# Kernel tuning notes

Measured on AMD Instinct MI355X. Metric: run time of the kernel, lower is better.

## Reference

```python
import jax, jax.numpy as jnp
import numpy as np

N = 16384          # num_nodes
B = 2              # batch_size
F = 32             # feature_size (hard-coded in module)
G = 16             # num_gru_units
OUT = 16           # output_dim


def _normalized_laplacian(adj):
    # calculate_laplacian_with_self_loop: D^-1/2 (A + I) D^-1/2
    a = adj + jnp.eye(adj.shape[0], dtype=adj.dtype)
    d = a.sum(axis=1)
    dinv = jax.lax.rsqrt(d)
    return dinv[:, None] * a * dinv[None, :]


def setup_inputs() -> dict:
    key = jax.random.key(0)
    k1, k2, k3, k4 = jax.random.split(key, 4)
    adj = (jax.random.uniform(k1, (N, N), dtype=jnp.float32) < 0.01).astype(jnp.float32)
    laplacian = _normalized_laplacian(adj)
    inputs = jax.random.normal(k2, (B, N, F), dtype=jnp.float32)
    hidden_state = jax.random.normal(k3, (B, N * G), dtype=jnp.float32)
    # xavier_uniform for weights [(G+F), OUT]
    limit = np.sqrt(6.0 / (G + F + OUT)).astype(np.float32)
    weights = jax.random.uniform(k4, (G + F, OUT), dtype=jnp.float32, minval=-limit, maxval=limit)
    biases = jnp.zeros((OUT,), dtype=jnp.float32)
    return {"inputs": inputs, "hidden_state": hidden_state, "laplacian": laplacian,
            "weights": weights, "biases": biases}


def reference(inputs, hidden_state, laplacian, weights, biases):
    b, n, f = inputs.shape
    g = weights.shape[0] - f
    out_dim = weights.shape[1]
    h = hidden_state.reshape(b, n, g)
    cat = jnp.concatenate([inputs, h], axis=2)              # [B, N, F+G]
    # laplacian @ concat over the node dimension (same math as the
    # reshape/transpose dance + per-batch sparse GEMM loop in the original)
    ax = jnp.einsum('mn,bnc->bmc', laplacian, cat)          # [B, N, F+G]
    out = ax @ weights + biases                             # [B, N, OUT]
    return out.reshape(b, n * out_dim)
```

## Files before the change

### kernel.cpp

```cpp
#include <hip/hip_runtime.h>
#include <hip/hip_bf16.h>


#define NN   16384
#define FF   32
#define GG   16
#define OUTD 16
#define C96  96
#define BM   64
#define BK   128
#define SPLITK 2
#define KCHUNK (NN / SPLITK)
#define KITERS (KCHUNK / BK)

typedef __attribute__((ext_vector_type(8))) short short8;
typedef __attribute__((ext_vector_type(4))) float f32x4;

using as1_void = __attribute__((address_space(1))) void;
using as3_void = __attribute__((address_space(3))) void;

__device__ __forceinline__ unsigned short f2bf(float f) {
  __hip_bfloat16 h = __float2bfloat16(f);
  return __builtin_bit_cast(unsigned short, h);
}

__global__ __launch_bounds__(256) void prep_xt(const float* __restrict__ inp,
                                               const float* __restrict__ hid,
                                               unsigned short* __restrict__ xt) {
  __shared__ float lds_cat[C96][64];
  const int tid = threadIdx.x;
  const int n0 = blockIdx.x * 64;

#pragma unroll
  for (int r = 0; r < 2; ++r) {
    int fi = tid + r * 256;
    int n = fi >> 3;
    int f4 = fi & 7;
#pragma unroll
    for (int b = 0; b < 2; ++b) {
      const float4* src = (const float4*)(inp + ((size_t)b * NN + (n0 + n)) * FF) + f4;
      float4 v = *src;
      int c = b * 48 + f4 * 4;
      lds_cat[c + 0][n] = v.x;
      lds_cat[c + 1][n] = v.y;
      lds_cat[c + 2][n] = v.z;
      lds_cat[c + 3][n] = v.w;
    }
  }
  {
    int n = tid >> 2;
    int g4 = tid & 3;
#pragma unroll
    for (int b = 0; b < 2; ++b) {
      const float4* src = (const float4*)(hid + ((size_t)b * NN + (n0 + n)) * GG) + g4;
      float4 v = *src;
      int c = b * 48 + 32 + g4 * 4;
      lds_cat[c + 0][n] = v.x;
      lds_cat[c + 1][n] = v.y;
      lds_cat[c + 2][n] = v.z;
      lds_cat[c + 3][n] = v.w;
    }
  }
  __syncthreads();
#pragma unroll
  for (int r = 0; r < 3; ++r) {
    int u = tid + r * 256;
    int c = u >> 3;
    int nn = (u & 7) * 8;
    short8 o;
#pragma unroll
    for (int j = 0; j < 8; ++j) o[j] = (short)f2bf(lds_cat[c][nn + j]);
    *(short8*)(xt + (size_t)c * NN + n0 + nn) = o;
  }
}

__global__ __launch_bounds__(256, 2) void spmm_main(const float* __restrict__ L,
                                                    const unsigned short* __restrict__ xt,
                                                    float* __restrict__ cp) {
  __shared__ __align__(16) float lds_a[BM * BK];
  __shared__ __align__(16) unsigned short lds_b[C96 * BK];

  const int tid = threadIdx.x;
  const int wave = tid >> 6;
  const int lane = tid & 63;
  const int m = lane & 15;
  const int quad = lane >> 4;
  const int sp = blockIdx.x & 1;
  const int m0 = (blockIdx.x >> 1) * BM;
  const int kb = sp * KCHUNK;

  const float* asrc[8];
  float* adst[8];
#pragma unroll
  for (int i = 0; i < 8; ++i) {
    int l = wave * 8 + i;
    int row = 2 * l + (lane >> 5);
    int cu = (lane & 31) ^ (row & 7);
    asrc[i] = L + (size_t)(m0 + row) * NN + kb + cu * 4;
    adst[i] = lds_a + l * 256;
  }
  const unsigned short* bsrc[6];
  unsigned short* bdst[6];
#pragma unroll
  for (int i = 0; i < 6; ++i) {
    int l = wave * 6 + i;
    int col = 4 * l + (lane >> 4);
    int cb = (lane & 15) ^ (col & 7);
    bsrc[i] = xt + (size_t)col * NN + kb + cb * 8;
    bdst[i] = lds_b + l * 512;
  }

  const int rowA = wave * 16 + m;
  int aoff[4][2];
#pragma unroll
  for (int kk = 0; kk < 4; ++kk) {
    int c0 = kk * 8 + quad * 2;
    aoff[kk][0] = (rowA * 32 + (c0 ^ (rowA & 7))) * 4;
    aoff[kk][1] = (rowA * 32 + ((c0 + 1) ^ (rowA & 7))) * 4;
  }
  int boff[4][6];
#pragma unroll
  for (int kk = 0; kk < 4; ++kk)
#pragma unroll
    for (int t = 0; t < 6; ++t) {
      int col = t * 16 + m;
      int u = kk * 4 + quad;
      boff[kk][t] = (col * 16 + (u ^ (col & 7))) * 8;
    }

  f32x4 acc[6];
#pragma unroll
  for (int t = 0; t < 6; ++t) acc[t] = (f32x4){0.f, 0.f, 0.f, 0.f};

  for (int it = 0; it < KITERS; ++it) {
    const int ko = it * BK;
#pragma unroll
    for (int i = 0; i < 8; ++i)
      __builtin_amdgcn_global_load_lds((const as1_void*)(asrc[i] + ko),
                                       (as3_void*)adst[i], 16, 0, 0);
#pragma unroll
    for (int i = 0; i < 6; ++i)
      __builtin_amdgcn_global_load_lds((const as1_void*)(bsrc[i] + ko),
                                       (as3_void*)bdst[i], 16, 0, 0);
    __syncthreads();

#pragma unroll
    for (int kk = 0; kk < 4; ++kk) {
      f32x4 a0 = *(const f32x4*)(lds_a + aoff[kk][0]);
      f32x4 a1 = *(const f32x4*)(lds_a + aoff[kk][1]);
      short8 af;
      af[0] = (short)f2bf(a0[0]); af[1] = (short)f2bf(a0[1]);
      af[2] = (short)f2bf(a0[2]); af[3] = (short)f2bf(a0[3]);
      af[4] = (short)f2bf(a1[0]); af[5] = (short)f2bf(a1[1]);
      af[6] = (short)f2bf(a1[2]); af[7] = (short)f2bf(a1[3]);
#pragma unroll
      for (int t = 0; t < 6; ++t) {
        short8 bf = *(const short8*)(lds_b + boff[kk][t]);
        acc[t] = __builtin_amdgcn_mfma_f32_16x16x32_bf16(af, bf, acc[t], 0, 0, 0);
      }
    }
    __syncthreads();
  }

  float* cpd = cp + ((size_t)sp * NN + m0) * C96;
#pragma unroll
  for (int t = 0; t < 6; ++t) {
    int col = t * 16 + m;
#pragma unroll
    for (int r = 0; r < 4; ++r) {
      int row = wave * 16 + quad * 4 + r;
      cpd[(size_t)row * C96 + col] = acc[t][r];
    }
  }
}

__global__ __launch_bounds__(256) void epilogue(const float* __restrict__ cp,
                                                const float* __restrict__ w,
                                                const float* __restrict__ bias,
                                                float* __restrict__ out) {
  __shared__ float lds_c[64 * 97];
  __shared__ float lds_w[48 * 16];
  __shared__ float lds_bias[16];
  const int tid = threadIdx.x;
  const int n0 = blockIdx.x * 64;

  for (int i = tid; i < 768; i += 256) lds_w[i] = w[i];
  if (tid < 16) lds_bias[tid] = bias[tid];

  const size_t base = (size_t)n0 * C96;
#pragma unroll
  for (int i = 0; i < 24; ++i) {
    int e = tid + i * 256;
    float s = 0.f;
#pragma unroll
    for (int sp = 0; sp < SPLITK; ++sp)
      s += cp[(size_t)sp * ((size_t)NN * C96) + base + e];
    lds_c[e + e / 96] = s;
  }
  __syncthreads();

  const int node = tid >> 2;
  const int b = (tid >> 1) & 1;
  const int o0 = (tid & 1) * 8;
  const float* crow_l = &lds_c[node * 97 + b * 48];
  float accv[8];
#pragma unroll
  for (int o = 0; o < 8; ++o) accv[o] = lds_bias[o0 + o];
#pragma unroll
  for (int j = 0; j < 48; ++j) {
    float cv = crow_l[j];
#pragma unroll
    for (int o = 0; o < 8; ++o) accv[o] += cv * lds_w[j * 16 + o0 + o];
  }
  size_t ob = (size_t)b * ((size_t)NN * OUTD) + (size_t)(n0 + node) * OUTD + o0;
  float4 v0 = {accv[0], accv[1], accv[2], accv[3]};
  float4 v1 = {accv[4], accv[5], accv[6], accv[7]};
  *(float4*)(out + ob) = v0;
  *(float4*)(out + ob + 4) = v1;
}

extern "C" void kernel_launch(void* const* d_in, const int* in_sizes, int n_in,
                              void* d_out, int out_size, void* d_ws, size_t ws_size,
                              hipStream_t stream) {
  (void)in_sizes; (void)n_in; (void)out_size; (void)ws_size;
  const float* inp = (const float*)d_in[0];
  const float* hid = (const float*)d_in[1];
  const float* lap = (const float*)d_in[2];
  const float* wts = (const float*)d_in[3];
  const float* bia = (const float*)d_in[4];
  float* out = (float*)d_out;

  unsigned short* xt = (unsigned short*)d_ws;
  float* cp = (float*)((char*)d_ws + (4u << 20));

  prep_xt<<<NN / 64, 256, 0, stream>>>(inp, hid, xt);
  spmm_main<<<(NN / BM) * SPLITK, 256, 0, stream>>>(lap, xt, cp);
  epilogue<<<NN / 64, 256, 0, stream>>>(cp, wts, bia, out);
}
```

Baseline: 1.411 ms.

## Double-buffer spmm LDS tiles with smaller K tile and 4-way split-K

Restructures the dense Laplacian GEMM main loop to prefetch the next K tile into a second LDS buffer while computing on the current one, so global-to-LDS loads overlap the MFMA work. The K tile shrinks from 128 to 32 and split-K grows from 2 to 4, which cuts LDS use and lets more blocks per CU be resident. The epilogue reads SPLITK partials, so it now reduces four partial buffers, adding traffic to the workspace. A single barrier per iteration orders buffer reuse, and the per-tile LDS layout and swizzle are rewritten to match.

```diff
diff --git a/kernel.cpp b/kernel.cpp
--- a/kernel.cpp
+++ b/kernel.cpp
@@ -8,8 +8,8 @@
 #define OUTD 16
 #define C96  96
 #define BM   64
-#define BK   128
-#define SPLITK 2
+#define BK   32
+#define SPLITK 4
 #define KCHUNK (NN / SPLITK)
 #define KITERS (KCHUNK / BK)
 
@@ -74,92 +74,114 @@
   }
 }
 
-__global__ __launch_bounds__(256, 2) void spmm_main(const float* __restrict__ L,
+__global__ __launch_bounds__(256, 4) void spmm_main(const float* __restrict__ L,
                                                     const unsigned short* __restrict__ xt,
                                                     float* __restrict__ cp) {
-  __shared__ __align__(16) float lds_a[BM * BK];
-  __shared__ __align__(16) unsigned short lds_b[C96 * BK];
+  __shared__ __align__(16) float lds_a[2][BM * 8 * 4];
+  __shared__ __align__(16) unsigned short lds_b[2][C96 * BK];
 
   const int tid = threadIdx.x;
   const int wave = tid >> 6;
   const int lane = tid & 63;
   const int m = lane & 15;
   const int quad = lane >> 4;
-  const int sp = blockIdx.x & 1;
-  const int m0 = (blockIdx.x >> 1) * BM;
+  const int bx = blockIdx.x;
+  const int sp = bx & 3;
+  const int m0 = (bx >> 2) * BM;
   const int kb = sp * KCHUNK;
 
-  const float* asrc[8];
-  float* adst[8];
-#pragma unroll
-  for (int i = 0; i < 8; ++i) {
-    int l = wave * 8 + i;
-    int row = 2 * l + (lane >> 5);
-    int cu = (lane & 31) ^ (row & 7);
+  const float* asrc[2];
+  float* adst0[2], *adst1[2];
+#pragma unroll
+  for (int i = 0; i < 2; ++i) {
+    int l = wave * 2 + i;
+    int s = l * 64 + lane;
+    int row = s >> 3;
+    int cu = (s & 7) ^ (row & 7);
     asrc[i] = L + (size_t)(m0 + row) * NN + kb + cu * 4;
-    adst[i] = lds_a + l * 256;
-  }
-  const unsigned short* bsrc[6];
-  unsigned short* bdst[6];
-#pragma unroll
-  for (int i = 0; i < 6; ++i) {
-    int l = wave * 6 + i;
-    int col = 4 * l + (lane >> 4);
-    int cb = (lane & 15) ^ (col & 7);
-    bsrc[i] = xt + (size_t)col * NN + kb + cb * 8;
-    bdst[i] = lds_b + l * 512;
+    adst0[i] = &lds_a[0][l * 256];
+    adst1[i] = &lds_a[1][l * 256];
+  }
+  const unsigned short* bsrc[2];
+  unsigned short* bdst0[2], *bdst1[2];
+  const bool has_b = (wave < 3);
+  if (has_b) {
+#pragma unroll
+    for (int i = 0; i < 2; ++i) {
+      int t = wave * 2 + i;
+      int col = t * 16 + m;
+      int u = quad;
+      bsrc[i] = xt + (size_t)col * NN + kb + u * 8;
+      bdst0[i] = &lds_b[0][t * 512];
+      bdst1[i] = &lds_b[1][t * 512];
+    }
   }
 
   const int rowA = wave * 16 + m;
-  int aoff[4][2];
-#pragma unroll
-  for (int kk = 0; kk < 4; ++kk) {
-    int c0 = kk * 8 + quad * 2;
-    aoff[kk][0] = (rowA * 32 + (c0 ^ (rowA & 7))) * 4;
-    aoff[kk][1] = (rowA * 32 + ((c0 + 1) ^ (rowA & 7))) * 4;
-  }
-  int boff[4][6];
-#pragma unroll
-  for (int kk = 0; kk < 4; ++kk)
+  const int aoff0 = (rowA * 8 + ((quad * 2) ^ (rowA & 7))) * 4;
+  const int aoff1 = (rowA * 8 + ((quad * 2 + 1) ^ (rowA & 7))) * 4;
+  int boff[6];
+#pragma unroll
+  for (int t = 0; t < 6; ++t)
+    boff[t] = (t * 64 + quad * 16 + m) * 8;
+
+  f32x4 acc[6];
+#pragma unroll
+  for (int t = 0; t < 6; ++t) acc[t] = (f32x4){0.f, 0.f, 0.f, 0.f};
+
+#pragma unroll
+  for (int i = 0; i < 2; ++i)
+    __builtin_amdgcn_global_load_lds((const as1_void*)asrc[i],
+                                     (as3_void*)adst0[i], 16, 0, 0);
+  if (has_b) {
+#pragma unroll
+    for (int i = 0; i < 2; ++i)
+      __builtin_amdgcn_global_load_lds((const as1_void*)bsrc[i],
+                                       (as3_void*)bdst0[i], 16, 0, 0);
+  }
+
+  for (int it = 0; it < KITERS; ++it) {
+    __syncthreads();
+
+    if (it + 1 < KITERS) {
+      const int ko = (it + 1) * BK;
+      if ((it & 1) == 0) {
+#pragma unroll
+        for (int i = 0; i < 2; ++i)
+          __builtin_amdgcn_global_load_lds((const as1_void*)(asrc[i] + ko),
+                                           (as3_void*)adst1[i], 16, 0, 0);
+        if (has_b)
+#pragma unroll
+          for (int i = 0; i < 2; ++i)
+            __builtin_amdgcn_global_load_lds((const as1_void*)(bsrc[i] + ko),
+                                             (as3_void*)bdst1[i], 16, 0, 0);
+      } else {
+#pragma unroll
+        for (int i = 0; i < 2; ++i)
+          __builtin_amdgcn_global_load_lds((const as1_void*)(asrc[i] + ko),
+                                           (as3_void*)adst0[i], 16, 0, 0);
+        if (has_b)
+#pragma unroll
+          for (int i = 0; i < 2; ++i)
+            __builtin_amdgcn_global_load_lds((const as1_void*)(bsrc[i] + ko),
+                                             (as3_void*)bdst0[i], 16, 0, 0);
+      }
+    }
+
+    const float* ab = lds_a[it & 1];
+    const unsigned short* bb = lds_b[it & 1];
+    f32x4 a0 = *(const f32x4*)(ab + aoff0);
+    f32x4 a1 = *(const f32x4*)(ab + aoff1);
+    short8 af;
+    af[0] = (short)f2bf(a0[0]); af[1] = (short)f2bf(a0[1]);
+    af[2] = (short)f2bf(a0[2]); af[3] = (short)f2bf(a0[3]);
+    af[4] = (short)f2bf(a1[0]); af[5] = (short)f2bf(a1[1]);
+    af[6] = (short)f2bf(a1[2]); af[7] = (short)f2bf(a1[3]);
 #pragma unroll
     for (int t = 0; t < 6; ++t) {
-      int col = t * 16 + m;
-      int u = kk * 4 + quad;
-      boff[kk][t] = (col * 16 + (u ^ (col & 7))) * 8;
-    }
-
-  f32x4 acc[6];
-#pragma unroll
-  for (int t = 0; t < 6; ++t) acc[t] = (f32x4){0.f, 0.f, 0.f, 0.f};
-
-  for (int it = 0; it < KITERS; ++it) {
-    const int ko = it * BK;
-#pragma unroll
-    for (int i = 0; i < 8; ++i)
-      __builtin_amdgcn_global_load_lds((const as1_void*)(asrc[i] + ko),
-                                       (as3_void*)adst[i], 16, 0, 0);
-#pragma unroll
-    for (int i = 0; i < 6; ++i)
-      __builtin_amdgcn_global_load_lds((const as1_void*)(bsrc[i] + ko),
-                                       (as3_void*)bdst[i], 16, 0, 0);
-    __syncthreads();
-
-#pragma unroll
-    for (int kk = 0; kk < 4; ++kk) {
-      f32x4 a0 = *(const f32x4*)(lds_a + aoff[kk][0]);
-      f32x4 a1 = *(const f32x4*)(lds_a + aoff[kk][1]);
-      short8 af;
-      af[0] = (short)f2bf(a0[0]); af[1] = (short)f2bf(a0[1]);
-      af[2] = (short)f2bf(a0[2]); af[3] = (short)f2bf(a0[3]);
-      af[4] = (short)f2bf(a1[0]); af[5] = (short)f2bf(a1[1]);
-      af[6] = (short)f2bf(a1[2]); af[7] = (short)f2bf(a1[3]);
-#pragma unroll
-      for (int t = 0; t < 6; ++t) {
-        short8 bf = *(const short8*)(lds_b + boff[kk][t]);
-        acc[t] = __builtin_amdgcn_mfma_f32_16x16x32_bf16(af, bf, acc[t], 0, 0, 0);
-      }
-    }
-    __syncthreads();
+      short8 bf = *(const short8*)(bb + boff[t]);
+      acc[t] = __builtin_amdgcn_mfma_f32_16x16x32_bf16(af, bf, acc[t], 0, 0, 0);
+    }
   }
 
   float* cpd = cp + ((size_t)sp * NN + m0) * C96;
```

New measurement: 1.393 ms. About the same (-1.3%).
